# Optimization experiments

Hardware: AMD Instinct MI355X
Metric: run time of the kernel (lower is better)

## Reference

```python
import jax, jax.numpy as jnp
import numpy as np

FEAT = 256
L = 8          # max_evi_length (chain length)
MC = 8         # max_chain
N = 4096       # examples
B = N * MC


def setup_inputs() -> dict:
    key = jax.random.key(0)
    ks = jax.random.split(key, 8)
    x = jax.random.normal(ks[0], (B, L, FEAT), dtype=jnp.float32)
    # end_inds: one-hot float indicator of chain end position (>=1)
    pos = jax.random.randint(ks[1], (B,), 1, L)
    end_inds = jax.nn.one_hot(pos, L, dtype=jnp.float32)
    s_in = 1.0 / np.sqrt(2 * FEAT)
    s_d = 1.0 / np.sqrt(FEAT)
    Wc = jax.random.uniform(ks[2], (FEAT, 2 * FEAT), minval=-s_in, maxval=s_in, dtype=jnp.float32)
    bc = jax.random.uniform(ks[3], (FEAT,), minval=-s_in, maxval=s_in, dtype=jnp.float32)
    Wcs = jax.random.uniform(ks[4], (FEAT, FEAT), minval=-s_d, maxval=s_d, dtype=jnp.float32)
    Wanti = jax.random.uniform(ks[5], (FEAT, 2 * FEAT), minval=-s_in, maxval=s_in, dtype=jnp.float32)
    Wout = jax.random.uniform(ks[6], (2, 2 * FEAT), minval=-s_in, maxval=s_in, dtype=jnp.float32)
    bout = jax.random.uniform(ks[7], (2,), minval=-s_in, maxval=s_in, dtype=jnp.float32)
    return dict(x=x, end_inds=end_inds, max_chain=MC, Wc=Wc, bc=bc,
                Wcs=Wcs, Wanti=Wanti, Wout=Wout, bout=bout)


def _forward(x, end_inds, max_chain, Wc, bc, Wcs, Wanti, Wout, bout):
    Bx, Lx, d = x.shape
    h_c0 = jnp.swapaxes(x[:, :-1, :], 0, 1)   # [L-1, B, d]
    h_e0 = jnp.swapaxes(x[:, 1:, :], 0, 1)    # [L-1, B, d]
    # anti_updater(cat([h_c0, h_e0])) precomputed (depends only on x)
    anti = jnp.concatenate([h_c0, h_e0], -1) @ Wanti.T  # [L-1, B, d]
    s0 = x[:, 0, :]                           # initial s_anti

    def step(s, inp):
        hc0, he0, a = inp
        # note: original uses state_updater_c for BOTH h_c and h_e
        h_c = jnp.concatenate([s, hc0], -1) @ Wc.T + bc
        h_e = jnp.concatenate([s, he0], -1) @ Wc.T + bc
        cs = jax.nn.sigmoid(jnp.sum((h_c @ Wcs.T) * h_e, -1))  # [B]
        s_new = jnp.tanh(cs[:, None] * a) + s
        return s_new, (cs, s_new)

    _, (cs_ls, s_ls) = jax.lax.scan(step, s0, (h_c0, h_e0, anti))
    cs_ls = cs_ls.T                    # [B, L-1]
    s_ls = jnp.swapaxes(s_ls, 0, 1)    # [B, L-1, d]

    cum_cs = jnp.cumprod(cs_ls, axis=-1)
    ei = end_inds[:, 1:]               # [B, L-1]
    cum = (cum_cs * ei).sum(-1) - (1.0 - ei.sum(-1)) * 10000.0
    cum = jax.nn.softmax(cum.reshape(-1, max_chain), axis=-1)   # [N, MC]

    s_sel = (s_ls * ei[:, :, None]).sum(1)           # [B, d]
    s_sel = s_sel.reshape(-1, max_chain, d)          # [N, MC, d]
    u = jnp.einsum('nmd,nm->nd', s_sel, cum)         # bmm over chains
    u = jnp.concatenate([x[::max_chain, 0], u], -1)  # [N, 2d]
    return u @ Wout.T + bout                         # [N, 2]


def reference(x, end_inds, max_chain, Wc, bc, Wcs, Wanti, Wout, bout):
    return _forward(x, end_inds, max_chain, Wc, bc, Wcs, Wanti, Wout, bout)
```

## Files before the change

### kernel.cpp

```cpp
#include <hip/hip_runtime.h>

#define FEATN 256
#define XROW  2048
#define MT    64
#define NW    16
#define LDST  264
#define TILE  (MT * LDST)
#define NSTEP 7

using f32x4 = __attribute__((ext_vector_type(4))) float;
using s16x8 = __attribute__((ext_vector_type(8))) short;

__device__ __forceinline__ short f2bf(float f) {
  unsigned u = __float_as_uint(f);
  u += 0x7fffu + ((u >> 16) & 1u);
  return (short)(u >> 16);
}

__device__ __forceinline__ f32x4 ntload4(const float* p) {
  return __builtin_nontemporal_load(reinterpret_cast<const f32x4*>(p));
}

__device__ __forceinline__ s16x8 pack8(const f32x4 a, const f32x4 b) {
  s16x8 r;
  r[0] = f2bf(a[0]); r[1] = f2bf(a[1]); r[2] = f2bf(a[2]); r[3] = f2bf(a[3]);
  r[4] = f2bf(b[0]); r[5] = f2bf(b[1]); r[6] = f2bf(b[2]); r[7] = f2bf(b[3]);
  return r;
}

__global__ void prep_kernel(const float* __restrict__ Wc, const float* __restrict__ bc,
                            const float* __restrict__ Wcs, const float* __restrict__ Wanti,
                            short* __restrict__ Wt, float* __restrict__ bq) {
  __shared__ float wrow[FEATN];
  __shared__ float red[FEATN];
  const int n = blockIdx.x, k = threadIdx.x;
  wrow[k] = Wcs[n * FEATN + k];
  __syncthreads();
  float a0 = 0.f, a1 = 0.f;
  #pragma unroll 8
  for (int j = 0; j < FEATN; ++j) {
    const float w = wrow[j];
    a0 += w * Wc[j * 512 + k];
    a1 += w * Wc[j * 512 + 256 + k];
  }
  red[k] = wrow[k] * bc[k];
  __syncthreads();
  for (int off = 128; off > 0; off >>= 1) {
    if (k < off) red[k] += red[k + off];
    __syncthreads();
  }
  if (k == 0) bq[n] = red[0];
  const int fo = (n >> 4) * 4096 + (k >> 5) * 512 + (((k >> 3) & 3) * 16 + (n & 15)) * 8 + (k & 7);
  Wt[0 * 65536 + fo] = f2bf(a0);
  Wt[1 * 65536 + fo] = f2bf(a1);
  Wt[2 * 65536 + fo] = f2bf(Wc[n * 512 + k]);
  Wt[3 * 65536 + fo] = f2bf(Wc[n * 512 + 256 + k]);
  Wt[4 * 65536 + fo] = f2bf(Wanti[n * 512 + k]);
  Wt[5 * 65536 + fo] = f2bf(Wanti[n * 512 + 256 + k]);
}

__global__ __launch_bounds__(1024, 4)
void chain_kernel(const float* __restrict__ x, const float* __restrict__ endi,
                  const short* __restrict__ Wt, const float* __restrict__ bq,
                  const float* __restrict__ bc, const float* __restrict__ Wout,
                  const float* __restrict__ bout, float* __restrict__ out) {
  __shared__ short sbuf[2 * TILE];
  __shared__ float redP[MT][NW];
  __shared__ float selP[MT][2 * NW];
  __shared__ float cpL[MT], cumL[MT], seL[MT], csL[MT], eiL[MT];

  const int tid  = (int)threadIdx.x;
  const int lane = tid & 63;
  const int wave = tid >> 6;
  const int lr   = lane & 15;
  const int lh   = lane >> 4;
  const int r0   = (int)blockIdx.x * MT;

  if (tid < MT) { cpL[tid] = 1.f; cumL[tid] = 0.f; seL[tid] = 0.f; }
  #pragma unroll
  for (int i = 0; i < 2; ++i) (&selP[0][0])[i * 1024 + tid] = 0.f;

  #pragma unroll
  for (int i = 0; i < 2; ++i) {
    const int f = i * 8192 + tid * 8;
    const int row = f >> 8, col = f & 255;
    const float* src = &x[(size_t)(r0 + row) * XROW + col];
    const s16x8 b = pack8(ntload4(src), ntload4(src + 4));
    *reinterpret_cast<s16x8*>(&sbuf[row * LDST + col]) = b;
    *reinterpret_cast<s16x8*>(&sbuf[TILE + row * LDST + col]) = b;
  }

  const int wcol = wave * 16 + lr;
  const short* wfb = Wt + wave * 4096 + lane * 8;
  const int abase = lr * LDST + lh * 8;
  const float bqv = bq[wcol];
  const float bcv = bc[wcol];
  const float wo0 = Wout[256 + wcol];
  const float wo1 = Wout[768 + wcol];
  const f32x4 fzero = {0.f, 0.f, 0.f, 0.f};

  float sreg[4][4];
  #pragma unroll
  for (int m = 0; m < 4; ++m)
    #pragma unroll
    for (int e = 0; e < 4; ++e)
      sreg[m][e] = x[(size_t)(r0 + m * 16 + lh * 4 + e) * XROW + wcol];

  __syncthreads();

  for (int t = 0; t < NSTEP; ++t) {
    const int so = (t & 1) * TILE;
    const int xo = ((t + 1) & 1) * TILE;

    f32x4 AccA[4], AccB[4], AccN[4];
    #pragma unroll
    for (int m = 0; m < 4; ++m) { AccA[m] = fzero; AccB[m] = fzero; AccN[m] = fzero; }

    #pragma unroll 1
    for (int ks = 0; ks < 8; ++ks) {
      const short* p = wfb + ks * 512;
      {
        const s16x8 b0 = *reinterpret_cast<const s16x8*>(p + 0 * 65536);
        const s16x8 b2 = *reinterpret_cast<const s16x8*>(p + 2 * 65536);
        #pragma unroll
        for (int m = 0; m < 4; ++m) {
          const s16x8 a_s = *reinterpret_cast<const s16x8*>(&sbuf[so + abase + m * (16 * LDST) + ks * 32]);
          AccA[m] = __builtin_amdgcn_mfma_f32_16x16x32_bf16(a_s, b0, AccA[m], 0, 0, 0);
          AccB[m] = __builtin_amdgcn_mfma_f32_16x16x32_bf16(a_s, b2, AccB[m], 0, 0, 0);
        }
      }
      {
        const s16x8 b1 = *reinterpret_cast<const s16x8*>(p + 1 * 65536);
        const s16x8 b4 = *reinterpret_cast<const s16x8*>(p + 4 * 65536);
        #pragma unroll
        for (int m = 0; m < 4; ++m) {
          const s16x8 a_x = *reinterpret_cast<const s16x8*>(&sbuf[xo + abase + m * (16 * LDST) + ks * 32]);
          AccA[m] = __builtin_amdgcn_mfma_f32_16x16x32_bf16(a_x, b1, AccA[m], 0, 0, 0);
          AccN[m] = __builtin_amdgcn_mfma_f32_16x16x32_bf16(a_x, b4, AccN[m], 0, 0, 0);
        }
      }
    }
    __syncthreads();

    #pragma unroll
    for (int i = 0; i < 2; ++i) {
      const int f = i * 8192 + tid * 8;
      const int row = f >> 8, col = f & 255;
      const float* src = &x[(size_t)(r0 + row) * XROW + (t + 1) * FEATN + col];
      const s16x8 b = pack8(ntload4(src), ntload4(src + 4));
      *reinterpret_cast<s16x8*>(&sbuf[so + row * LDST + col]) = b;
    }
    __syncthreads();

    #pragma unroll 1
    for (int ks = 0; ks < 8; ++ks) {
      const short* p = wfb + ks * 512;
      const s16x8 b3 = *reinterpret_cast<const s16x8*>(p + 3 * 65536);
      const s16x8 b5 = *reinterpret_cast<const s16x8*>(p + 5 * 65536);
      #pragma unroll
      for (int m = 0; m < 4; ++m) {
        const s16x8 a_n = *reinterpret_cast<const s16x8*>(&sbuf[so + abase + m * (16 * LDST) + ks * 32]);
        AccB[m] = __builtin_amdgcn_mfma_f32_16x16x32_bf16(a_n, b3, AccB[m], 0, 0, 0);
        AccN[m] = __builtin_amdgcn_mfma_f32_16x16x32_bf16(a_n, b5, AccN[m], 0, 0, 0);
      }
    }

    #pragma unroll
    for (int m = 0; m < 4; ++m) {
      #pragma unroll
      for (int e = 0; e < 4; ++e) {
        float p = (AccA[m][e] + bqv) * (AccB[m][e] + bcv);
        p += __shfl_xor(p, 1);
        p += __shfl_xor(p, 2);
        p += __shfl_xor(p, 4);
        p += __shfl_xor(p, 8);
        if (lr == 0) redP[m * 16 + lh * 4 + e][wave] = p;
      }
    }
    __syncthreads();

    if (tid < MT) {
      float d = 0.f;
      #pragma unroll
      for (int w = 0; w < NW; ++w) d += redP[tid][w];
      const float cs = 1.f / (1.f + __expf(-d));
      const float cp = cpL[tid] * cs;
      cpL[tid] = cp;
      const float ei = endi[(size_t)(r0 + tid) * 8 + (t + 1)];
      cumL[tid] += cp * ei;
      seL[tid] += ei;
      csL[tid] = cs;
      eiL[tid] = ei;
    }
    __syncthreads();

    #pragma unroll
    for (int m = 0; m < 4; ++m) {
      #pragma unroll
      for (int e = 0; e < 4; ++e) {
        const int row = m * 16 + lh * 4 + e;
        const float cs = csL[row];
        const float ag = cs * AccN[m][e];
        const float ex = __expf(2.f * ag);
        const float th = 1.f - 2.f / (ex + 1.f);
        const float sn = sreg[m][e] + th;
        sreg[m][e] = sn;
        sbuf[xo + row * LDST + wcol] = f2bf(sn);
        if (eiL[row] != 0.f) {
          float p0 = sn * wo0;
          float p1 = sn * wo1;
          p0 += __shfl_xor(p0, 1); p0 += __shfl_xor(p0, 2);
          p0 += __shfl_xor(p0, 4); p0 += __shfl_xor(p0, 8);
          p1 += __shfl_xor(p1, 1); p1 += __shfl_xor(p1, 2);
          p1 += __shfl_xor(p1, 4); p1 += __shfl_xor(p1, 8);
          if (lr == 0) { selP[row][wave * 2] = p0; selP[row][wave * 2 + 1] = p1; }
        }
      }
    }
    __syncthreads();
  }

  if (wave < 8) {
    const int g = wave;
    const int rowb = g * 8;
    float c[8];
    float mx = -3.4e38f;
    #pragma unroll
    for (int m = 0; m < 8; ++m) {
      c[m] = cumL[rowb + m] - (1.f - seL[rowb + m]) * 10000.f;
      mx = fmaxf(mx, c[m]);
    }
    float sum = 0.f;
    float wgt[8];
    #pragma unroll
    for (int m = 0; m < 8; ++m) { wgt[m] = __expf(c[m] - mx); sum += wgt[m]; }
    const float inv = 1.f / sum;
    float up0 = 0.f, up1 = 0.f;
    #pragma unroll
    for (int m = 0; m < 8; ++m) {
      float s0 = 0.f, s1 = 0.f;
      #pragma unroll
      for (int w = 0; w < NW; ++w) {
        s0 += selP[rowb + m][w * 2];
        s1 += selP[rowb + m][w * 2 + 1];
      }
      const float wm = wgt[m] * inv;
      up0 += wm * s0; up1 += wm * s1;
    }
    const int d = lane * 4;
    const float4 xv  = *reinterpret_cast<const float4*>(&x[(size_t)(r0 + rowb) * XROW + d]);
    const float4 w00 = *reinterpret_cast<const float4*>(&Wout[d]);
    const float4 w10 = *reinterpret_cast<const float4*>(&Wout[512 + d]);
    float o0 = xv.x * w00.x + xv.y * w00.y + xv.z * w00.z + xv.w * w00.w;
    float o1 = xv.x * w10.x + xv.y * w10.y + xv.z * w10.z + xv.w * w10.w;
    #pragma unroll
    for (int off = 1; off < 64; off <<= 1) {
      o0 += __shfl_xor(o0, off);
      o1 += __shfl_xor(o1, off);
    }
    if (lane == 0) {
      const int n = (int)blockIdx.x * 8 + g;
      out[n * 2 + 0] = o0 + up0 + bout[0];
      out[n * 2 + 1] = o1 + up1 + bout[1];
    }
  }
}

extern "C" void kernel_launch(void* const* d_in, const int* in_sizes, int n_in,
                              void* d_out, int out_size, void* d_ws, size_t ws_size,
                              hipStream_t stream) {
  const float* x     = (const float*)d_in[0];
  const float* endi  = (const float*)d_in[1];
  const float* Wc    = (const float*)d_in[3];
  const float* bc    = (const float*)d_in[4];
  const float* Wcs   = (const float*)d_in[5];
  const float* Wanti = (const float*)d_in[6];
  const float* Wout  = (const float*)d_in[7];
  const float* bout  = (const float*)d_in[8];
  float* out = (float*)d_out;

  char* ws = (char*)d_ws;
  short* Wt = (short*)ws;
  float* bq = (float*)(ws + 786432);

  prep_kernel<<<dim3(256), dim3(256), 0, stream>>>(Wc, bc, Wcs, Wanti, Wt, bq);
  chain_kernel<<<dim3(512), dim3(1024), 0, stream>>>(x, endi, Wt, bq, bc, Wout, bout, out);
}
```

Measured before the change: 296.6 us.

## Switch recurrent GEMMs from 16x16x32 to 32x32x16 MFMA with 2x8 wave tiling

Retiles the per-step matmuls so each of the 16 waves owns a 32-row by 32-column output tile and uses 32x32x16 bf16 MFMAs instead of four 16x16x32 MFMAs over all 64 rows. The weight pre-layout is changed to match the new B-fragment order, and the row reductions and selection partials now span 8 column-waves with 32-lane shuffles. The aim is fewer LDS A-fragment loads per MFMA and fewer weight fragment reloads per wave, since each weight fragment now covers 32 rows. In exchange the reduction needs an extra shuffle stage, and the accumulator register layout changes.

```diff
diff --git a/kernel.cpp b/kernel.cpp
--- a/kernel.cpp
+++ b/kernel.cpp
@@ -3,13 +3,13 @@
 #define FEATN 256
 #define XROW  2048
 #define MT    64
-#define NW    16
 #define LDST  264
 #define TILE  (MT * LDST)
 #define NSTEP 7
 
-using f32x4 = __attribute__((ext_vector_type(4))) float;
-using s16x8 = __attribute__((ext_vector_type(8))) short;
+using f32x4  = __attribute__((ext_vector_type(4))) float;
+using f32x16 = __attribute__((ext_vector_type(16))) float;
+using s16x8  = __attribute__((ext_vector_type(8))) short;
 
 __device__ __forceinline__ short f2bf(float f) {
   unsigned u = __float_as_uint(f);
@@ -50,7 +50,7 @@
     __syncthreads();
   }
   if (k == 0) bq[n] = red[0];
-  const int fo = (n >> 4) * 4096 + (k >> 5) * 512 + (((k >> 3) & 3) * 16 + (n & 15)) * 8 + (k & 7);
+  const int fo = (n >> 5) * 8192 + (k >> 4) * 512 + (((k >> 3) & 1) * 32 + (n & 31)) * 8 + (k & 7);
   Wt[0 * 65536 + fo] = f2bf(a0);
   Wt[1 * 65536 + fo] = f2bf(a1);
   Wt[2 * 65536 + fo] = f2bf(Wc[n * 512 + k]);
@@ -65,20 +65,19 @@
                   const float* __restrict__ bc, const float* __restrict__ Wout,
                   const float* __restrict__ bout, float* __restrict__ out) {
   __shared__ short sbuf[2 * TILE];
-  __shared__ float redP[MT][NW];
-  __shared__ float selP[MT][2 * NW];
+  __shared__ float redP[MT][9];
+  __shared__ float selP[MT][17];
   __shared__ float cpL[MT], cumL[MT], seL[MT], csL[MT], eiL[MT];
 
   const int tid  = (int)threadIdx.x;
   const int lane = tid & 63;
   const int wave = tid >> 6;
-  const int lr   = lane & 15;
-  const int lh   = lane >> 4;
+  const int l5   = lane & 31;
+  const int h    = lane >> 5;
   const int r0   = (int)blockIdx.x * MT;
 
   if (tid < MT) { cpL[tid] = 1.f; cumL[tid] = 0.f; seL[tid] = 0.f; }
-  #pragma unroll
-  for (int i = 0; i < 2; ++i) (&selP[0][0])[i * 1024 + tid] = 0.f;
+  for (int i = tid; i < MT * 17; i += 1024) (&selP[0][0])[i] = 0.f;
 
   #pragma unroll
   for (int i = 0; i < 2; ++i) {
@@ -90,21 +89,22 @@
     *reinterpret_cast<s16x8*>(&sbuf[TILE + row * LDST + col]) = b;
   }
 
-  const int wcol = wave * 16 + lr;
-  const short* wfb = Wt + wave * 4096 + lane * 8;
-  const int abase = lr * LDST + lh * 8;
-  const float bqv = bq[wcol];
-  const float bcv = bc[wcol];
-  const float wo0 = Wout[256 + wcol];
-  const float wo1 = Wout[768 + wcol];
-  const f32x4 fzero = {0.f, 0.f, 0.f, 0.f};
-
-  float sreg[4][4];
+  const int wr  = (wave >> 3) * 32;
+  const int wc  = (wave & 7) * 32;
+  const int wcl = wc + l5;
+  const short* wfb = Wt + (wave & 7) * 8192 + lane * 8;
+  const int abase = (wr + l5) * LDST + h * 8;
+  const float bqv = bq[wcl];
+  const float bcv = bc[wcl];
+  const float wo0 = Wout[256 + wcl];
+  const float wo1 = Wout[768 + wcl];
+
+  float sreg[16];
   #pragma unroll
-  for (int m = 0; m < 4; ++m)
-    #pragma unroll
-    for (int e = 0; e < 4; ++e)
-      sreg[m][e] = x[(size_t)(r0 + m * 16 + lh * 4 + e) * XROW + wcol];
+  for (int e = 0; e < 16; ++e) {
+    const int row = wr + (e & 3) + 8 * (e >> 2) + 4 * h;
+    sreg[e] = x[(size_t)(r0 + row) * XROW + wcl];
+  }
 
   __syncthreads();
 
@@ -112,32 +112,26 @@
     const int so = (t & 1) * TILE;
     const int xo = ((t + 1) & 1) * TILE;
 
-    f32x4 AccA[4], AccB[4], AccN[4];
-    #pragma unroll
-    for (int m = 0; m < 4; ++m) { AccA[m] = fzero; AccB[m] = fzero; AccN[m] = fzero; }
+    f32x16 AccA, AccB, AccN;
+    #pragma unroll
+    for (int e = 0; e < 16; ++e) { AccA[e] = 0.f; AccB[e] = 0.f; AccN[e] = 0.f; }
 
     #pragma unroll 1
-    for (int ks = 0; ks < 8; ++ks) {
+    for (int ks = 0; ks < 16; ++ks) {
       const short* p = wfb + ks * 512;
       {
         const s16x8 b0 = *reinterpret_cast<const s16x8*>(p + 0 * 65536);
         const s16x8 b2 = *reinterpret_cast<const s16x8*>(p + 2 * 65536);
-        #pragma unroll
-        for (int m = 0; m < 4; ++m) {
-          const s16x8 a_s = *reinterpret_cast<const s16x8*>(&sbuf[so + abase + m * (16 * LDST) + ks * 32]);
-          AccA[m] = __builtin_amdgcn_mfma_f32_16x16x32_bf16(a_s, b0, AccA[m], 0, 0, 0);
-          AccB[m] = __builtin_amdgcn_mfma_f32_16x16x32_bf16(a_s, b2, AccB[m], 0, 0, 0);
-        }
+        const s16x8 a_s = *reinterpret_cast<const s16x8*>(&sbuf[so + abase + ks * 16]);
+        AccA = __builtin_amdgcn_mfma_f32_32x32x16_bf16(a_s, b0, AccA, 0, 0, 0);
+        AccB = __builtin_amdgcn_mfma_f32_32x32x16_bf16(a_s, b2, AccB, 0, 0, 0);
       }
       {
         const s16x8 b1 = *reinterpret_cast<const s16x8*>(p + 1 * 65536);
         const s16x8 b4 = *reinterpret_cast<const s16x8*>(p + 4 * 65536);
-        #pragma unroll
-        for (int m = 0; m < 4; ++m) {
-          const s16x8 a_x = *reinterpret_cast<const s16x8*>(&sbuf[xo + abase + m * (16 * LDST) + ks * 32]);
-          AccA[m] = __builtin_amdgcn_mfma_f32_16x16x32_bf16(a_x, b1, AccA[m], 0, 0, 0);
-          AccN[m] = __builtin_amdgcn_mfma_f32_16x16x32_bf16(a_x, b4, AccN[m], 0, 0, 0);
-        }
+        const s16x8 a_x = *reinterpret_cast<const s16x8*>(&sbuf[xo + abase + ks * 16]);
+        AccA = __builtin_amdgcn_mfma_f32_32x32x16_bf16(a_x, b1, AccA, 0, 0, 0);
+        AccN = __builtin_amdgcn_mfma_f32_32x32x16_bf16(a_x, b4, AccN, 0, 0, 0);
       }
     }
     __syncthreads();
@@ -153,36 +147,31 @@
     __syncthreads();
 
     #pragma unroll 1
-    for (int ks = 0; ks < 8; ++ks) {
+    for (int ks = 0; ks < 16; ++ks) {
       const short* p = wfb + ks * 512;
       const s16x8 b3 = *reinterpret_cast<const s16x8*>(p + 3 * 65536);
       const s16x8 b5 = *reinterpret_cast<const s16x8*>(p + 5 * 65536);
-      #pragma unroll
-      for (int m = 0; m < 4; ++m) {
-        const s16x8 a_n = *reinterpret_cast<const s16x8*>(&sbuf[so + abase + m * (16 * LDST) + ks * 32]);
-        AccB[m] = __builtin_amdgcn_mfma_f32_16x16x32_bf16(a_n, b3, AccB[m], 0, 0, 0);
-        AccN[m] = __builtin_amdgcn_mfma_f32_16x16x32_bf16(a_n, b5, AccN[m], 0, 0, 0);
-      }
-    }
-
-    #pragma unroll
-    for (int m = 0; m < 4; ++m) {
-      #pragma unroll
-      for (int e = 0; e < 4; ++e) {
-        float p = (AccA[m][e] + bqv) * (AccB[m][e] + bcv);
-        p += __shfl_xor(p, 1);
-        p += __shfl_xor(p, 2);
-        p += __shfl_xor(p, 4);
-        p += __shfl_xor(p, 8);
-        if (lr == 0) redP[m * 16 + lh * 4 + e][wave] = p;
-      }
+      const s16x8 a_n = *reinterpret_cast<const s16x8*>(&sbuf[so + abase + ks * 16]);
+      AccB = __builtin_amdgcn_mfma_f32_32x32x16_bf16(a_n, b3, AccB, 0, 0, 0);
+      AccN = __builtin_amdgcn_mfma_f32_32x32x16_bf16(a_n, b5, AccN, 0, 0, 0);
+    }
+
+    #pragma unroll
+    for (int e = 0; e < 16; ++e) {
+      float pp = (AccA[e] + bqv) * (AccB[e] + bcv);
+      pp += __shfl_xor(pp, 1);
+      pp += __shfl_xor(pp, 2);
+      pp += __shfl_xor(pp, 4);
+      pp += __shfl_xor(pp, 8);
+      pp += __shfl_xor(pp, 16);
+      if (l5 == 0) redP[wr + (e & 3) + 8 * (e >> 2) + 4 * h][wave & 7] = pp;
     }
     __syncthreads();
 
     if (tid < MT) {
       float d = 0.f;
       #pragma unroll
-      for (int w = 0; w < NW; ++w) d += redP[tid][w];
+      for (int w = 0; w < 8; ++w) d += redP[tid][w];
       const float cs = 1.f / (1.f + __expf(-d));
       const float cp = cpL[tid] * cs;
       cpL[tid] = cp;
@@ -195,26 +184,24 @@
     __syncthreads();
 
     #pragma unroll
-    for (int m = 0; m < 4; ++m) {
-      #pragma unroll
-      for (int e = 0; e < 4; ++e) {
-        const int row = m * 16 + lh * 4 + e;
-        const float cs = csL[row];
-        const float ag = cs * AccN[m][e];
-        const float ex = __expf(2.f * ag);
-        const float th = 1.f - 2.f / (ex + 1.f);
-        const float sn = sreg[m][e] + th;
-        sreg[m][e] = sn;
-        sbuf[xo + row * LDST + wcol] = f2bf(sn);
-        if (eiL[row] != 0.f) {
-          float p0 = sn * wo0;
-          float p1 = sn * wo1;
-          p0 += __shfl_xor(p0, 1); p0 += __shfl_xor(p0, 2);
-          p0 += __shfl_xor(p0, 4); p0 += __shfl_xor(p0, 8);
-          p1 += __shfl_xor(p1, 1); p1 += __shfl_xor(p1, 2);
-          p1 += __shfl_xor(p1, 4); p1 += __shfl_xor(p1, 8);
-          if (lr == 0) { selP[row][wave * 2] = p0; selP[row][wave * 2 + 1] = p1; }
-        }
+    for (int e = 0; e < 16; ++e) {
+      const int row = wr + (e & 3) + 8 * (e >> 2) + 4 * h;
+      const float cs = csL[row];
+      const float ag = cs * AccN[e];
+      const float ex = __expf(2.f * ag);
+      const float th = 1.f - 2.f / (ex + 1.f);
+      const float sn = sreg[e] + th;
+      sreg[e] = sn;
+      sbuf[xo + row * LDST + wcl] = f2bf(sn);
+      if (eiL[row] != 0.f) {
+        float p0 = sn * wo0;
+        float p1 = sn * wo1;
+        p0 += __shfl_xor(p0, 1);  p1 += __shfl_xor(p1, 1);
+        p0 += __shfl_xor(p0, 2);  p1 += __shfl_xor(p1, 2);
+        p0 += __shfl_xor(p0, 4);  p1 += __shfl_xor(p1, 4);
+        p0 += __shfl_xor(p0, 8);  p1 += __shfl_xor(p1, 8);
+        p0 += __shfl_xor(p0, 16); p1 += __shfl_xor(p1, 16);
+        if (l5 == 0) { selP[row][(wave & 7) * 2] = p0; selP[row][(wave & 7) * 2 + 1] = p1; }
       }
     }
     __syncthreads();
@@ -240,7 +227,7 @@
     for (int m = 0; m < 8; ++m) {
       float s0 = 0.f, s1 = 0.f;
       #pragma unroll
-      for (int w = 0; w < NW; ++w) {
+      for (int w = 0; w < 8; ++w) {
         s0 += selP[rowb + m][w * 2];
         s1 += selP[rowb + m][w * 2 + 1];
       }
```

New measurement: 363.6 us. 1.23x slower.
